# Performance work log

Measured on AMD Instinct MI355X. Metric: run time of the kernel, lower is better.

## Reference

```python
import jax, jax.numpy as jnp
import numpy as np

HIDDEN = 2048
N_HEADS = 16
N_KV = 4
HEAD_DIM = 128
B, T = 2, 2048


def setup_inputs() -> dict:
    key = jax.random.key(0)
    k1, k2, k3, k4 = jax.random.split(key, 4)
    x = jax.random.normal(k1, (B, T, HIDDEN), dtype=jnp.float32)
    # linear weights stored [out, in] like torch; we apply x @ W.T
    w_q = jax.random.normal(k2, (N_HEADS * HEAD_DIM, HIDDEN), dtype=jnp.float32) * (HIDDEN ** -0.5)
    w_kv = jax.random.normal(k3, (2 * N_KV * HEAD_DIM, HIDDEN), dtype=jnp.float32) * (HIDDEN ** -0.5)
    w_o = jax.random.normal(k4, (HIDDEN, N_HEADS * HEAD_DIM), dtype=jnp.float32) * ((N_HEADS * HEAD_DIM) ** -0.5)
    return {"x": x, "w_q": w_q, "w_kv": w_kv, "w_o": w_o}


def reference(x, w_q, w_kv, w_o):
    b, t, _ = x.shape
    groups = N_HEADS // N_KV
    scale = HEAD_DIM ** -0.5

    q = (x @ w_q.T).reshape(b, t, N_HEADS, HEAD_DIM).transpose(0, 2, 1, 3)  # [B,H,T,D]
    kv = x @ w_kv.T
    k, v = jnp.split(kv, 2, axis=-1)
    k = k.reshape(b, t, N_KV, HEAD_DIM).transpose(0, 2, 1, 3)  # [B,KV,T,D]
    v = v.reshape(b, t, N_KV, HEAD_DIM).transpose(0, 2, 1, 3)
    # repeat_interleave over head dim -> [B,H,T,D]
    k = jnp.repeat(k, groups, axis=1)
    v = jnp.repeat(v, groups, axis=1)

    scores = jnp.einsum('bhqd,bhkd->bhqk', q, k) * scale  # [B,H,T,T]
    causal = jnp.triu(jnp.ones((t, t), dtype=bool), k=1)
    scores = jnp.where(causal, -jnp.inf, scores)
    weights = jax.nn.softmax(scores, axis=-1)
    out = jnp.einsum('bhqk,bhkd->bhqd', weights, v)  # [B,H,T,D]
    out = out.transpose(0, 2, 1, 3).reshape(b, t, N_HEADS * HEAD_DIM)
    return out @ w_o.T
```

## Files before the change

### kernel.cpp

```cpp
#include <hip/hip_runtime.h>

typedef short bf16x8 __attribute__((ext_vector_type(8)));
typedef float f32x4 __attribute__((ext_vector_type(4)));
typedef unsigned int u32x4 __attribute__((ext_vector_type(4)));

__device__ __forceinline__ unsigned short f2bf(float f) {
    unsigned int u = __float_as_uint(f);
    u = (u + 0x7fff + ((u >> 16) & 1)) >> 16;
    return (unsigned short)u;
}
__device__ __forceinline__ float bf2f(short s) {
    return __uint_as_float(((unsigned int)(unsigned short)s) << 16);
}

__device__ __forceinline__ void async16(const void* g, void* l) {
    __builtin_amdgcn_global_load_lds(
        (const __attribute__((address_space(1))) void*)g,
        (__attribute__((address_space(3))) void*)l,
        16 , 0 , 0 );
}

__global__ __launch_bounds__(256) void castall(const float* __restrict__ x,
                                               const float* __restrict__ wq,
                                               const float* __restrict__ wkv,
                                               const float* __restrict__ wo,
                                               unsigned short* __restrict__ xb,
                                               unsigned short* __restrict__ wqkvb,
                                               unsigned short* __restrict__ wob) {
    int i = blockIdx.x * blockDim.x + threadIdx.x;
    const float* src; unsigned short* dst; int j;
    if (i < 2097152)      { src = x;   dst = xb;    j = i; }
    else if (i < 3145728) { src = wq;  dst = wqkvb; j = i - 2097152; }
    else if (i < 3670016) { src = wkv; dst = wqkvb + (size_t)2048 * 2048; j = i - 3145728; }
    else                  { src = wo;  dst = wob;   j = i - 3670016; }
    float4 f = ((const float4*)src)[j];
    ushort4 u;
    u.x = f2bf(f.x); u.y = f2bf(f.y); u.z = f2bf(f.z); u.w = f2bf(f.w);
    ((ushort4*)dst)[j] = u;
}

template <int NREP, typename OutT>
__global__ __launch_bounds__(512, 2) void gemm8p(const unsigned short* __restrict__ A,
                                                 const unsigned short* __restrict__ B,
                                                 OutT* __restrict__ C,
                                                 unsigned short* __restrict__ VtOut,
                                                 int N, int K, int NT,
                                                 int ncut, float qscale) {
    constexpr int NCH = 4 + NREP;
    __shared__ __attribute__((aligned(16))) unsigned short LA[2][256 * 64];
    __shared__ __attribute__((aligned(16))) unsigned short LB[2][NREP * 64 * 64];

    const int tid  = threadIdx.x;
    const int lane = tid & 63;
    const int w    = tid >> 6;
    const int quad = lane >> 4;
    const int l16  = lane & 15;
    const int wm   = w >> 2;
    const int wn   = w & 3;

    const int lid = blockIdx.x + (int)gridDim.x * blockIdx.y;
    const int xcd = lid & 7, idx = lid >> 3;
    const int bx  = (xcd & 3) * 4 + (idx & 3);
    const int by  = (xcd >> 2) * 8 + (idx >> 2);
    const int m0  = bx * 256;
    const int n0  = by * (NREP * 64);
    const int swz = (l16 & 7) << 3;

    const int lr = lane >> 3;
    const int ls = lane & 7;
    const int ss = ls ^ lr;
    const unsigned short* aSrc = A + (size_t)(m0 + w * 8 + lr) * K + ss * 8;
    const unsigned short* bSrc = B + (size_t)(n0 + w * 8 + lr) * K + ss * 8;

    f32x4 acc[8][NREP] = {};

    auto stage1 = [&](int nb, int t, int si) {
        if (si >= NCH) return;
        if (si < NREP) {
            async16(bSrc + (size_t)si * 64 * K + t * 64, &LB[nb][(si * 64 + w * 8) * 64]);
        } else {
            int j = si - NREP;
            int c = (j == 0) ? 0 : (j == 1) ? 2 : (j == 2) ? 1 : 3;
            async16(aSrc + (size_t)c * 64 * K + t * 64, &LA[nb][(c * 64 + w * 8) * 64]);
        }
    };

    auto phase = [&](int cur, int q, bf16x8 (&bf)[NREP][2], int tn, bool last) {
        bf16x8 af[2][2];
        if (q == 0) {
#pragma unroll
            for (int n = 0; n < NREP; ++n)
#pragma unroll
                for (int kk = 0; kk < 2; ++kk)
                    bf[n][kk] = *(const bf16x8*)&LB[cur][(size_t)(wn * (NREP * 16) + n * 16 + l16) * 64
                                                         + ((kk * 32 + quad * 8) ^ swz)];
        }
#pragma unroll
        for (int mi = 0; mi < 2; ++mi)
#pragma unroll
            for (int kk = 0; kk < 2; ++kk)
                af[mi][kk] = *(const bf16x8*)&LA[cur][(size_t)(wm * 128 + (q * 2 + mi) * 16 + l16) * 64
                                                      + ((kk * 32 + quad * 8) ^ swz)];
        if (!last) { stage1(cur ^ 1, tn, 2 * q); stage1(cur ^ 1, tn, 2 * q + 1); }
        if (q == 1) {
            if (last) asm volatile("s_waitcnt vmcnt(0)" ::: "memory");
            else      asm volatile("s_waitcnt vmcnt(4)" ::: "memory");
        }
        if (q == 3 && !last) asm volatile("s_waitcnt vmcnt(2)" ::: "memory");
        __builtin_amdgcn_s_barrier();
        asm volatile("s_waitcnt lgkmcnt(0)" ::: "memory");
        __builtin_amdgcn_sched_barrier(0);
        __builtin_amdgcn_s_setprio(1);
#pragma unroll
        for (int mi = 0; mi < 2; ++mi)
#pragma unroll
            for (int n = 0; n < NREP; ++n)
#pragma unroll
                for (int kk = 0; kk < 2; ++kk)
                    acc[q * 2 + mi][n] = __builtin_amdgcn_mfma_f32_16x16x32_bf16(
                        af[mi][kk], bf[n][kk], acc[q * 2 + mi][n], 0, 0, 0);
        __builtin_amdgcn_s_setprio(0);
        __builtin_amdgcn_s_barrier();
    };

    auto ktile = [&](int cur, int tn, bool last) {
        bf16x8 bf[NREP][2];
        phase(cur, 0, bf, tn, last);
        phase(cur, 1, bf, tn, last);
        phase(cur, 2, bf, tn, last);
        phase(cur, 3, bf, tn, last);
    };

#pragma unroll
    for (int s = 0; s < NCH; ++s) stage1(0, 0, s);
    asm volatile("s_waitcnt vmcnt(2)" ::: "memory");
    __builtin_amdgcn_s_barrier();

    int cur = 0;
    for (int t = 0; t < NT - 1; ++t) {
        ktile(cur, t + 1, false);
        cur ^= 1;
    }
    ktile(cur, 0, true);

#pragma unroll
    for (int m = 0; m < 8; ++m) {
        int row = m0 + wm * 128 + m * 16 + quad * 4;
#pragma unroll
        for (int n = 0; n < NREP; ++n) {
            int col = n0 + wn * (NREP * 16) + n * 16 + l16;
            f32x4 v = acc[m][n];
            float s = (col < ncut) ? qscale : 1.0f;
            if (VtOut != nullptr && col >= 2560) {
                int bb = row >> 11, t0 = row & 2047;
                ushort4 o;
                o.x = f2bf(v[0]); o.y = f2bf(v[1]); o.z = f2bf(v[2]); o.w = f2bf(v[3]);
                *(ushort4*)(VtOut + ((size_t)(bb * 512 + (col - 2560))) * 2048 + t0) = o;
            } else {
#pragma unroll
                for (int j = 0; j < 4; ++j) {
                    float vj = v[j] * s;
                    if constexpr (sizeof(OutT) == 4)
                        C[(size_t)(row + j) * N + col] = vj;
                    else
                        C[(size_t)(row + j) * N + col] = f2bf(vj);
                }
            }
        }
    }
}

__global__ __launch_bounds__(256, 2) void attn_fwd9(const unsigned short* __restrict__ QKV,
                                                    const unsigned short* __restrict__ Vt,
                                                    unsigned short* __restrict__ Opart,
                                                    float* __restrict__ lpart) {
    __shared__ __attribute__((aligned(16))) unsigned short Ks[64 * 128];
    __shared__ __attribute__((aligned(16))) unsigned short Vs[2][128 * 64];

    const int tid  = threadIdx.x;
    const int lane = tid & 63;
    const int w    = tid >> 6;
    const int quad = lane >> 4;
    const int l16  = lane & 15;
    const int swz  = (l16 & 7) << 3;

    const int hb   = blockIdx.x;
    const int h    = hb & 15;
    const int b    = hb >> 4;
    const int y    = blockIdx.y;
    const int p    = 15 - (y >> 1);
    const int half = y & 1;
    const int kvh  = h >> 2;
    const float M_FIX = 12.0f;

    const int ntot   = p + 1;
    const int tstart = half ? ntot : 0;
    const int tend   = half ? 2 * ntot : ntot;

    const int qbase = p * 128;
    const int qw0   = qbase + w * 32;
    const int qw1   = qw0 + 16;

    bf16x8 qf[2][4];
#pragma unroll
    for (int g = 0; g < 2; ++g)
#pragma unroll
        for (int kd = 0; kd < 4; ++kd)
            qf[g][kd] = *(const bf16x8*)(QKV + (size_t)(b * 2048 + qw0 + g * 16 + l16) * 3072
                                         + h * 128 + kd * 32 + quad * 8);

    f32x4 oacc[2][8] = {};
    f32x4 rs4[2] = {};

    const unsigned short* gk[4];
    const unsigned short* gv[4];
#pragma unroll
    for (int pp = 0; pp < 4; ++pp) {
        int r  = (4 * w + pp) * 4 + (lane >> 4);
        int s  = lane & 15;
        int sp = (s & 8) | ((s ^ r) & 7);
        gk[pp] = QKV + (size_t)(b * 2048 + r) * 3072 + 2048 + kvh * 128 + sp * 8;
        int d  = (4 * w + pp) * 8 + (lane >> 3);
        int sv = (lane & 7) ^ (d & 7);
        gv[pp] = Vt + ((size_t)(b * 4 + kvh) * 128 + d) * 2048 + sv * 8;
    }

    auto stageK = [&](int t) {
        const size_t ko = (size_t)t * 64;
#pragma unroll
        for (int pp = 0; pp < 4; ++pp)
            async16(gk[pp] + ko * 3072, &Ks[(4 * w + pp) * 512]);
    };
    auto stageV = [&](int nb, int t) {
        const size_t ko = (size_t)t * 64;
#pragma unroll
        for (int pp = 0; pp < 4; ++pp)
            async16(gv[pp] + ko, &Vs[nb][(4 * w + pp) * 512]);
    };

    stageK(tstart);
    stageV(0, tstart);
    int cur = 0;

    for (int t = tstart; t < tend; ++t) {
        __syncthreads();
        if (t + 1 < tend) stageV(cur ^ 1, t + 1);
        const int k0 = t * 64;
        const bool liveW = (k0 <= qw0 + 15);
        const bool live1 = (k0 <= qw1 + 15);

        bf16x8 pa[2][2];
        if (liveW) {
            f32x4 sacc[2][4] = {};
            __builtin_amdgcn_s_setprio(1);
#pragma unroll
            for (int kt = 0; kt < 4; ++kt) {
                bf16x8 kf[4];
#pragma unroll
                for (int kd = 0; kd < 4; ++kd)
                    kf[kd] = *(const bf16x8*)&Ks[(kt * 16 + l16) * 128
                                                 + ((kd * 32 + quad * 8) ^ swz)];
#pragma unroll
                for (int kd = 0; kd < 4; ++kd)
                    sacc[0][kt] = __builtin_amdgcn_mfma_f32_16x16x32_bf16(kf[kd], qf[0][kd], sacc[0][kt], 0, 0, 0);
                if (live1) {
#pragma unroll
                    for (int kd = 0; kd < 4; ++kd)
                        sacc[1][kt] = __builtin_amdgcn_mfma_f32_16x16x32_bf16(kf[kd], qf[1][kd], sacc[1][kt], 0, 0, 0);
                }
            }
            __builtin_amdgcn_s_setprio(0);

#pragma unroll
            for (int g = 0; g < 2; ++g) {
                if (g == 1 && !live1) continue;
                const int qwg  = qw0 + g * 16;
                const bool diag = (k0 + 63 > qwg);
                const int qrow = qwg + l16;
                unsigned int pk[4][2];
#pragma unroll
                for (int kt = 0; kt < 4; ++kt) {
                    float pvv[4];
#pragma unroll
                    for (int j = 0; j < 4; ++j) {
                        float pv = __expf(sacc[g][kt][j] - M_FIX);
                        if (diag) {
                            int key = k0 + kt * 16 + quad * 4 + j;
                            if (key > qrow) pv = 0.f;
                        }
                        rs4[g][j] += pv;
                        pvv[j] = pv;
                    }
                    asm("v_cvt_pk_bf16_f32 %0, %1, %2" : "=v"(pk[kt][0]) : "v"(pvv[0]), "v"(pvv[1]));
                    asm("v_cvt_pk_bf16_f32 %0, %1, %2" : "=v"(pk[kt][1]) : "v"(pvv[2]), "v"(pvv[3]));
                }
#pragma unroll
                for (int ks = 0; ks < 2; ++ks) {
                    unsigned int d0 = pk[2 * ks][0], s0 = pk[2 * ks + 1][0];
                    unsigned int d1 = pk[2 * ks][1], s1 = pk[2 * ks + 1][1];
                    asm("v_permlane32_swap_b32 %0, %1" : "+v"(d0), "+v"(s0));
                    asm("v_permlane16_swap_b32 %0, %1" : "+v"(d0), "+v"(s0));
                    asm("v_permlane32_swap_b32 %0, %1" : "+v"(d1), "+v"(s1));
                    asm("v_permlane16_swap_b32 %0, %1" : "+v"(d1), "+v"(s1));
                    u32x4 tt;
                    tt.x = d0;
                    tt.y = d1;
                    tt.z = s0;
                    tt.w = s1;
                    pa[g][ks] = __builtin_bit_cast(bf16x8, tt);
                }
            }
        }

        asm volatile("s_waitcnt lgkmcnt(0)" ::: "memory");
        __builtin_amdgcn_s_barrier();
        if (t + 1 < tend) stageK(t + 1);

        if (liveW) {
            __builtin_amdgcn_s_setprio(1);
#pragma unroll
            for (int dt = 0; dt < 8; ++dt) {
                bf16x8 vf[2];
#pragma unroll
                for (int ks = 0; ks < 2; ++ks)
                    vf[ks] = *(const bf16x8*)&Vs[cur][(dt * 16 + l16) * 64
                                                      + ((ks * 32 + quad * 8) ^ swz)];
#pragma unroll
                for (int ks = 0; ks < 2; ++ks)
                    oacc[0][dt] = __builtin_amdgcn_mfma_f32_16x16x32_bf16(pa[0][ks], vf[ks], oacc[0][dt], 0, 0, 0);
                if (live1) {
#pragma unroll
                    for (int ks = 0; ks < 2; ++ks)
                        oacc[1][dt] = __builtin_amdgcn_mfma_f32_16x16x32_bf16(pa[1][ks], vf[ks], oacc[1][dt], 0, 0, 0);
                }
            }
            __builtin_amdgcn_s_setprio(0);
        }
        cur ^= 1;
    }

#pragma unroll
    for (int g = 0; g < 2; ++g) {
        float r = (rs4[g][0] + rs4[g][1]) + (rs4[g][2] + rs4[g][3]);
        r += __shfl_xor(r, 16, 64);
        r += __shfl_xor(r, 32, 64);
        if (lane < 16)
            lpart[((size_t)(half * 2 + b) * 16 + h) * 2048 + qw0 + g * 16 + lane] = r;
#pragma unroll
        for (int dt = 0; dt < 8; ++dt)
#pragma unroll
            for (int j = 0; j < 4; ++j) {
                int qrow = qw0 + g * 16 + quad * 4 + j;
                Opart[(size_t)(half * 4096 + b * 2048 + qrow) * 2048 + h * 128 + dt * 16 + l16] =
                    f2bf(oacc[g][dt][j]);
            }
    }
}

__global__ __launch_bounds__(256) void combine(const unsigned short* __restrict__ Opart,
                                               const float* __restrict__ lpart,
                                               unsigned short* __restrict__ O) {
    const int r   = blockIdx.x;
    const int b   = r >> 11, row = r & 2047;
    const int col = threadIdx.x * 8;
    const int h   = col >> 7;
    bf16x8 a = *(const bf16x8*)(Opart + (size_t)r * 2048 + col);
    bf16x8 c = *(const bf16x8*)(Opart + (size_t)(4096 + r) * 2048 + col);
    float la = lpart[((size_t)(0 * 2 + b) * 16 + h) * 2048 + row];
    float lb = lpart[((size_t)(1 * 2 + b) * 16 + h) * 2048 + row];
    float inv = 1.0f / (la + lb);
    bf16x8 o;
#pragma unroll
    for (int i = 0; i < 8; ++i)
        o[i] = (short)f2bf((bf2f(a[i]) + bf2f(c[i])) * inv);
    *(bf16x8*)(O + (size_t)r * 2048 + col) = o;
}

extern "C" void kernel_launch(void* const* d_in, const int* in_sizes, int n_in,
                              void* d_out, int out_size, void* d_ws, size_t ws_size,
                              hipStream_t stream) {
    const float* x   = (const float*)d_in[0];
    const float* wq  = (const float*)d_in[1];
    const float* wkv = (const float*)d_in[2];
    const float* wo  = (const float*)d_in[3];
    float* out = (float*)d_out;

    char* ws = (char*)d_ws;
    size_t off = 0;
    auto alloc = [&](size_t bytes) { size_t o = off; off += (bytes + 255) & ~(size_t)255; return o; };
    unsigned short* xb    = (unsigned short*)(ws + alloc((size_t)4096 * 2048 * 2));
    unsigned short* wqkvb = (unsigned short*)(ws + alloc((size_t)3072 * 2048 * 2));
    unsigned short* wob   = (unsigned short*)(ws + alloc((size_t)2048 * 2048 * 2));
    unsigned short* QKVb  = (unsigned short*)(ws + alloc((size_t)4096 * 3072 * 2));
    unsigned short* Ab    = (unsigned short*)(ws + alloc((size_t)4096 * 2048 * 2));
    unsigned short* Vtb   = (unsigned short*)(ws + alloc((size_t)2 * 4 * 128 * 2048 * 2));
    unsigned short* Opart = (unsigned short*)(ws + alloc((size_t)2 * 4096 * 2048 * 2));
    float*          lpart = (float*)(ws + alloc((size_t)2 * 2 * 16 * 2048 * 4));

    const float qscale = 0.08838834764831845f;

    castall<<<18432, 256, 0, stream>>>(x, wq, wkv, wo, xb, wqkvb, wob);

    gemm8p<3, unsigned short><<<dim3(16, 16), 512, 0, stream>>>(xb, wqkvb, QKVb, Vtb,
                                                                3072, 2048, 32, 2048, qscale);

    attn_fwd9<<<dim3(32, 32), 256, 0, stream>>>(QKVb, Vtb, Opart, lpart);
    combine<<<4096, 256, 0, stream>>>(Opart, lpart, Ab);

    gemm8p<2, float><<<dim3(16, 16), 512, 0, stream>>>(Ab, wob, out, nullptr,
                                                       2048, 2048, 32, 0, 1.0f);
}
```

Measured before the change: 273.4 us.

## Fuse split-KV combine into attention via atomic last-arriver flag

Removes the separate combine kernel. Each attention block bumps an atomic counter per (head, query tile) after writing its partial output and row sums. The block that arrives second reads the other half's partial from global memory and writes the normalized final output. This saves one kernel launch and one full read and write pass over the combined output, at the cost of a threadfence, an atomic, and uncoalesced partial reads in the tail of half the blocks. The flags are cleared in the cast kernel.

```diff
diff --git a/kernel.cpp b/kernel.cpp
--- a/kernel.cpp
+++ b/kernel.cpp
@@ -26,7 +26,12 @@
                                                const float* __restrict__ wo,
                                                unsigned short* __restrict__ xb,
                                                unsigned short* __restrict__ wqkvb,
-                                               unsigned short* __restrict__ wob) {
+                                               unsigned short* __restrict__ wob,
+                                               unsigned int* __restrict__ flags) {
+    if (blockIdx.x == 0) {
+        flags[threadIdx.x] = 0u;
+        flags[threadIdx.x + 256] = 0u;
+    }
     int i = blockIdx.x * blockDim.x + threadIdx.x;
     const float* src; unsigned short* dst; int j;
     if (i < 2097152)      { src = x;   dst = xb;    j = i; }
@@ -170,12 +175,15 @@
     }
 }
 
-__global__ __launch_bounds__(256, 2) void attn_fwd9(const unsigned short* __restrict__ QKV,
-                                                    const unsigned short* __restrict__ Vt,
-                                                    unsigned short* __restrict__ Opart,
-                                                    float* __restrict__ lpart) {
+__global__ __launch_bounds__(256, 2) void attn_fwd12(const unsigned short* __restrict__ QKV,
+                                                     const unsigned short* __restrict__ Vt,
+                                                     unsigned short* __restrict__ Opart,
+                                                     float* __restrict__ lpart,
+                                                     unsigned int* __restrict__ flags,
+                                                     unsigned short* __restrict__ O) {
     __shared__ __attribute__((aligned(16))) unsigned short Ks[64 * 128];
     __shared__ __attribute__((aligned(16))) unsigned short Vs[2][128 * 64];
+    __shared__ int sflag;
 
     const int tid  = threadIdx.x;
     const int lane = tid & 63;
@@ -339,11 +347,13 @@
         cur ^= 1;
     }
 
+    float rown[2];
 #pragma unroll
     for (int g = 0; g < 2; ++g) {
         float r = (rs4[g][0] + rs4[g][1]) + (rs4[g][2] + rs4[g][3]);
         r += __shfl_xor(r, 16, 64);
         r += __shfl_xor(r, 32, 64);
+        rown[g] = r;
         if (lane < 16)
             lpart[((size_t)(half * 2 + b) * 16 + h) * 2048 + qw0 + g * 16 + lane] = r;
 #pragma unroll
@@ -355,25 +365,31 @@
                     f2bf(oacc[g][dt][j]);
             }
     }
-}
-
-__global__ __launch_bounds__(256) void combine(const unsigned short* __restrict__ Opart,
-                                               const float* __restrict__ lpart,
-                                               unsigned short* __restrict__ O) {
-    const int r   = blockIdx.x;
-    const int b   = r >> 11, row = r & 2047;
-    const int col = threadIdx.x * 8;
-    const int h   = col >> 7;
-    bf16x8 a = *(const bf16x8*)(Opart + (size_t)r * 2048 + col);
-    bf16x8 c = *(const bf16x8*)(Opart + (size_t)(4096 + r) * 2048 + col);
-    float la = lpart[((size_t)(0 * 2 + b) * 16 + h) * 2048 + row];
-    float lb = lpart[((size_t)(1 * 2 + b) * 16 + h) * 2048 + row];
-    float inv = 1.0f / (la + lb);
-    bf16x8 o;
-#pragma unroll
-    for (int i = 0; i < 8; ++i)
-        o[i] = (short)f2bf((bf2f(a[i]) + bf2f(c[i])) * inv);
-    *(bf16x8*)(O + (size_t)r * 2048 + col) = o;
+
+    __threadfence();
+    if (tid == 0) sflag = (int)atomicAdd(&flags[hb * 16 + p], 1u);
+    __syncthreads();
+    if (sflag == 1) {
+        __threadfence();
+        const int oh = half ^ 1;
+#pragma unroll
+        for (int g = 0; g < 2; ++g) {
+#pragma unroll
+            for (int j = 0; j < 4; ++j) {
+                int qrow = qw0 + g * 16 + quad * 4 + j;
+                float lo  = lpart[((size_t)(oh * 2 + b) * 16 + h) * 2048 + qrow];
+                float inv = 1.0f / (__shfl(rown[g], quad * 4 + j, 64) + lo);
+#pragma unroll
+                for (int dt = 0; dt < 8; ++dt) {
+                    float po   = bf2f((short)Opart[(size_t)(oh * 4096 + b * 2048 + qrow) * 2048
+                                                   + h * 128 + dt * 16 + l16]);
+                    float mine = bf2f((short)f2bf(oacc[g][dt][j]));
+                    O[(size_t)(b * 2048 + qrow) * 2048 + h * 128 + dt * 16 + l16] =
+                        f2bf((mine + po) * inv);
+                }
+            }
+        }
+    }
 }
 
 extern "C" void kernel_launch(void* const* d_in, const int* in_sizes, int n_in,
@@ -396,16 +412,16 @@
     unsigned short* Vtb   = (unsigned short*)(ws + alloc((size_t)2 * 4 * 128 * 2048 * 2));
     unsigned short* Opart = (unsigned short*)(ws + alloc((size_t)2 * 4096 * 2048 * 2));
     float*          lpart = (float*)(ws + alloc((size_t)2 * 2 * 16 * 2048 * 4));
+    unsigned int*   flags = (unsigned int*)(ws + alloc((size_t)512 * 4));
 
     const float qscale = 0.08838834764831845f;
 
-    castall<<<18432, 256, 0, stream>>>(x, wq, wkv, wo, xb, wqkvb, wob);
+    castall<<<18432, 256, 0, stream>>>(x, wq, wkv, wo, xb, wqkvb, wob, flags);
 
     gemm8p<3, unsigned short><<<dim3(16, 16), 512, 0, stream>>>(xb, wqkvb, QKVb, Vtb,
                                                                 3072, 2048, 32, 2048, qscale);
 
-    attn_fwd9<<<dim3(32, 32), 256, 0, stream>>>(QKVb, Vtb, Opart, lpart);
-    combine<<<4096, 256, 0, stream>>>(Opart, lpart, Ab);
+    attn_fwd12<<<dim3(32, 32), 256, 0, stream>>>(QKVb, Vtb, Opart, lpart, flags, Ab);
 
     gemm8p<2, float><<<dim3(16, 16), 512, 0, stream>>>(Ab, wob, out, nullptr,
                                                        2048, 2048, 32, 0, 1.0f);
```

New measurement: 491.1 us. 79.6% more time.
